# Performance work log

Hardware: AMD Instinct MI355X
Metric: run time of the kernel (lower is better)

The kernel has to match this reference:

```python
import jax, jax.numpy as jnp
import numpy as np

B, NBANDS, NCHAN, NTIME = 32, 9, 64, 4096
M = 32
C = M * NBANDS          # 288 spectral-spatial channels
SF = 4                  # strideFactor
TLEN = 2 * SF - 1       # 7 overlapping temporal windows
E = 2                   # embed_dim
H = 2                   # num_heads (head_dim = 1)
NCLASS = 4
BN_EPS = 1e-5


def _renorm(w, maxnorm):
    # torch.renorm(p=2, dim=0): clamp L2 norm of each dim-0 slice to maxnorm
    norms = jnp.sqrt(jnp.sum(w.reshape(w.shape[0], -1) ** 2, axis=1))
    scale = jnp.minimum(1.0, maxnorm / jnp.maximum(norms, 1e-7))
    return w * scale.reshape((-1,) + (1,) * (w.ndim - 1))


def _pos_embed():
    # get_1d_sincos_pos_embed_from_grid(embed_dim=2, len=7)
    pos = np.arange(TLEN, dtype=np.float32)
    omega = 1.0 / (10000.0 ** (np.arange(E // 2, dtype=np.float32) / (E / 2.0)))
    out = pos[:, None] * omega[None, :]
    return jnp.asarray(np.concatenate([np.sin(out), np.cos(out)], axis=1), jnp.float32)  # [TLEN, E]


def setup_inputs() -> dict:
    key = jax.random.key(0)
    ks = jax.random.split(key, 10)
    s = 0.1
    return {
        "x": jax.random.uniform(ks[0], (B, NBANDS, NCHAN, NTIME), jnp.float32),
        "conv_w": jax.random.normal(ks[1], (C, 1, NCHAN, 1), jnp.float32) * s,
        "conv_b": jax.random.normal(ks[2], (C,), jnp.float32) * s,
        "bn_gamma": jnp.ones((C,), jnp.float32),
        "bn_beta": jnp.zeros((C,), jnp.float32),
        "bn_mean": jnp.zeros((C,), jnp.float32),
        "bn_var": jnp.ones((C,), jnp.float32),
        "in_proj_w": jax.random.normal(ks[3], (C, 3 * E, E), jnp.float32) * s,
        "in_proj_b": jax.random.normal(ks[4], (C, 3 * E), jnp.float32) * s,
        "out_proj_w": jax.random.normal(ks[5], (C, E, E), jnp.float32) * s,
        "out_proj_b": jax.random.normal(ks[6], (C, E), jnp.float32) * s,
        "last_w": jax.random.normal(ks[7], (NCLASS, C * TLEN * E), jnp.float32) * s,
        "last_b": jax.random.normal(ks[8], (NCLASS,), jnp.float32) * s,
    }


def _forward(x, conv_w, conv_b, bn_gamma, bn_beta, bn_mean, bn_var,
             in_proj_w, in_proj_b, out_proj_w, out_proj_b, last_w, last_b):
    # --- SCB: grouped conv (nChan,1) + BatchNorm(eval) + swish ---
    w = _renorm(conv_w, 2.0)
    y = jax.lax.conv_general_dilated(
        x, w, window_strides=(1, 1), padding='VALID',
        dimension_numbers=('NCHW', 'OIHW', 'NCHW'),
        feature_group_count=NBANDS) + conv_b[None, :, None, None]      # [B,C,1,NTIME]
    y = (y - bn_mean[None, :, None, None]) * jax.lax.rsqrt(bn_var + BN_EPS)[None, :, None, None]
    y = y * bn_gamma[None, :, None, None] + bn_beta[None, :, None, None]
    y = y * jax.nn.sigmoid(y)  # swish

    # --- overlapping temporal windows stacked on dim 2 ---
    ts = NTIME // (SF * 2)
    xs = jnp.concatenate([y[:, :, :, i * ts:(i + 2) * ts] for i in range(TLEN)], axis=2)  # [B,C,TLEN,2ts]

    # --- tempo_layer: log-var, RMS/mean shape factor ---
    var = jnp.log(jnp.clip(jnp.var(xs, axis=3, keepdims=True, ddof=1), 1e-6, 1e6))
    mean_ = jnp.mean(xs, axis=3, keepdims=True)
    x_rms = jnp.sqrt(jnp.mean(xs ** 2, axis=3, keepdims=True))
    feat = jnp.concatenate([var, x_rms / mean_], axis=3)               # [B,C,TLEN,E]

    # --- batched per-channel multihead self-attention (replaces C-way loop) ---
    yq = feat + _pos_embed()[None, None]                               # [B,C,T,E]
    qkv = jnp.einsum('bcte,cfe->bctf', yq, in_proj_w) + in_proj_b[None, :, None, :]
    q, k, v = jnp.split(qkv, 3, axis=3)
    hd = E // H
    q = q.reshape(B, C, TLEN, H, hd)
    k = k.reshape(B, C, TLEN, H, hd)
    v = v.reshape(B, C, TLEN, H, hd)
    scores = jnp.einsum('bcthd,bcshd->bchts', q, k) / jnp.sqrt(jnp.float32(hd))
    att = jax.nn.softmax(scores, axis=-1)
    o = jnp.einsum('bchts,bcshd->bcthd', att, v).reshape(B, C, TLEN, E)
    o = jnp.einsum('bcte,cfe->bctf', o, out_proj_w) + out_proj_b[None, :, None, :]

    # --- classifier with weight-norm constraint + log-softmax ---
    flat = o.reshape(B, C * TLEN * E)
    lw = _renorm(last_w, 0.5)
    logits = flat @ lw.T + last_b
    return jax.nn.log_softmax(logits, axis=1)


def reference(x, conv_w, conv_b, bn_gamma, bn_beta, bn_mean, bn_var,
              in_proj_w, in_proj_b, out_proj_w, out_proj_b, last_w, last_b):
    return _forward(x, conv_w, conv_b, bn_gamma, bn_beta, bn_mean, bn_var,
                    in_proj_w, in_proj_b, out_proj_w, out_proj_b, last_w, last_b)
```

## Files before the change

### kernel.cpp

```cpp
#include <hip/hip_runtime.h>
#include <math.h>

#define BB     32
#define NBANDS 9
#define NCHAN  64
#define NTIME  4096
#define CC     288
#define TLEN   7
#define NSEG   8
#define SEGLEN 512
#define NCLASS 4

#define WS_WF    0
#define WS_BIAS  (WS_WF + CC*NCHAN)
#define WS_S1    (WS_BIAS + CC)
#define WS_S2    (WS_S1 + BB*CC*NSEG)
#define WS_FLAT  (WS_S2 + BB*CC*NSEG)

typedef _Float16 f16;
typedef __attribute__((ext_vector_type(8))) _Float16 f16x8;
typedef __attribute__((ext_vector_type(4))) float floatx4;

__global__ __launch_bounds__(64) void k0_fold(
    const float* __restrict__ cw, const float* __restrict__ cb,
    const float* __restrict__ gam, const float* __restrict__ bet,
    const float* __restrict__ mu, const float* __restrict__ var,
    f16* __restrict__ Wh, f16* __restrict__ Wl, float* __restrict__ biasf) {
  int c = blockIdx.x;
  int h = threadIdx.x;
  int g = c >> 5, cc = c & 31;
  float w = cw[c * NCHAN + h];
  float sq = w * w;
#pragma unroll
  for (int off = 32; off; off >>= 1) sq += __shfl_down(sq, off, 64);
  sq = __shfl(sq, 0, 64);
  float norm = sqrtf(sq);
  float scale = fminf(1.0f, 2.0f / fmaxf(norm, 1e-7f));
  float bns = gam[c] / sqrtf(var[c] + 1e-5f);
  float wf = w * scale * bns;
  f16 hi = (f16)wf;
  f16 lo = (f16)(wf - (float)hi);
  int o = g * (NCHAN * 32) + h * 32 + cc;
  Wh[o] = hi;
  Wl[o] = lo;
  if (h == 0) biasf[c] = (cb[c] - mu[c]) * bns + bet[c];
}

__global__ __launch_bounds__(256, 2) void k1_conv(
    const float* __restrict__ x, const f16* __restrict__ Wh,
    const f16* __restrict__ Wl, const float* __restrict__ biasf,
    float* __restrict__ S1, float* __restrict__ S2) {
  int gid = blockIdx.x;
  int seg = gid & 7;
  int g = (gid >> 3) % NBANDS;
  int b = gid / (NBANDS * NSEG);
  int tid = threadIdx.x;
  int wave = tid >> 6, lane = tid & 63;
  int quad = lane >> 4, li = lane & 15;

  const float* xp = x + (size_t)(b * NBANDS + g) * NCHAN * NTIME;
  const f16* wh = Wh + g * (NCHAN * 32);
  const f16* wl = Wl + g * (NCHAN * 32);

  f16x8 ah[2][2], al[2][2];
#pragma unroll
  for (int mt = 0; mt < 2; ++mt)
#pragma unroll
    for (int kb = 0; kb < 2; ++kb)
#pragma unroll
      for (int j = 0; j < 8; ++j) {
        int idx = (kb * 32 + quad * 8 + j) * 32 + mt * 16 + li;
        ah[mt][kb][j] = wh[idx];
        al[mt][kb][j] = wl[idx];
      }

  float biasr[2][4];
#pragma unroll
  for (int mt = 0; mt < 2; ++mt)
#pragma unroll
    for (int r = 0; r < 4; ++r)
      biasr[mt][r] = biasf[g * 32 + mt * 16 + quad * 4 + r];

  float s1a[2][4], s2a[2][4];
#pragma unroll
  for (int mt = 0; mt < 2; ++mt)
#pragma unroll
    for (int r = 0; r < 4; ++r) { s1a[mt][r] = 0.0f; s2a[mt][r] = 0.0f; }

#pragma unroll 1
  for (int ch = 0; ch < 2; ++ch) {
    int tc = seg * SEGLEN + wave * 128 + ch * 64;
    float4 v4[2][8];
#pragma unroll
    for (int kb = 0; kb < 2; ++kb)
#pragma unroll
      for (int j = 0; j < 8; ++j)
        v4[kb][j] = *(const float4*)(xp + (size_t)(kb * 32 + quad * 8 + j) * NTIME
                                     + tc + li * 4);
#pragma unroll
    for (int tau = 0; tau < 4; ++tau) {
      f16x8 bh[2], bl[2];
#pragma unroll
      for (int kb = 0; kb < 2; ++kb)
#pragma unroll
        for (int j = 0; j < 8; ++j) {
          float v = ((const float*)&v4[kb][j])[tau];
          f16 hi = (f16)v;
          bh[kb][j] = hi;
          bl[kb][j] = (f16)(v - (float)hi);
        }
      floatx4 acc0 = {0.0f, 0.0f, 0.0f, 0.0f};
      floatx4 acc1 = {0.0f, 0.0f, 0.0f, 0.0f};
#pragma unroll
      for (int kb = 0; kb < 2; ++kb) {
        acc0 = __builtin_amdgcn_mfma_f32_16x16x32_f16(ah[0][kb], bh[kb], acc0, 0, 0, 0);
        acc0 = __builtin_amdgcn_mfma_f32_16x16x32_f16(ah[0][kb], bl[kb], acc0, 0, 0, 0);
        acc0 = __builtin_amdgcn_mfma_f32_16x16x32_f16(al[0][kb], bh[kb], acc0, 0, 0, 0);
        acc1 = __builtin_amdgcn_mfma_f32_16x16x32_f16(ah[1][kb], bh[kb], acc1, 0, 0, 0);
        acc1 = __builtin_amdgcn_mfma_f32_16x16x32_f16(ah[1][kb], bl[kb], acc1, 0, 0, 0);
        acc1 = __builtin_amdgcn_mfma_f32_16x16x32_f16(al[1][kb], bh[kb], acc1, 0, 0, 0);
      }
#pragma unroll
      for (int r = 0; r < 4; ++r) {
        float d0 = acc0[r] + biasr[0][r];
        float d1 = acc1[r] + biasr[1][r];
        float y0 = d0 * __builtin_amdgcn_rcpf(1.0f + __expf(-d0));
        float y1 = d1 * __builtin_amdgcn_rcpf(1.0f + __expf(-d1));
        s1a[0][r] += y0; s2a[0][r] = fmaf(y0, y0, s2a[0][r]);
        s1a[1][r] += y1; s2a[1][r] = fmaf(y1, y1, s2a[1][r]);
      }
    }
  }

#pragma unroll
  for (int off = 8; off; off >>= 1) {
#pragma unroll
    for (int mt = 0; mt < 2; ++mt)
#pragma unroll
      for (int r = 0; r < 4; ++r) {
        s1a[mt][r] += __shfl_down(s1a[mt][r], off, 16);
        s2a[mt][r] += __shfl_down(s2a[mt][r], off, 16);
      }
  }

  __shared__ float part[2][32][4];
  if (li == 0) {
#pragma unroll
    for (int mt = 0; mt < 2; ++mt)
#pragma unroll
      for (int r = 0; r < 4; ++r) {
        int c = mt * 16 + quad * 4 + r;
        part[0][c][wave] = s1a[mt][r];
        part[1][c][wave] = s2a[mt][r];
      }
  }
  __syncthreads();
  if (tid < 64) {
    int c = tid >> 1, which = tid & 1;
    float v = part[which][c][0] + part[which][c][1] +
              part[which][c][2] + part[which][c][3];
    size_t o = (size_t)((b * CC) + g * 32 + c) * NSEG + seg;
    if (which == 0) S1[o] = v; else S2[o] = v;
  }
}

__global__ __launch_bounds__(256) void k2_attn(
    const float* __restrict__ S1, const float* __restrict__ S2,
    const float* __restrict__ ipw, const float* __restrict__ ipb,
    const float* __restrict__ opw, const float* __restrict__ opb,
    float* __restrict__ flat) {
  const float PSIN[TLEN] = {0.0f, 0.8414709848f, 0.9092974268f, 0.1411200081f,
                            -0.7568024953f, -0.9589242747f, -0.2794154982f};
  const float PCOS[TLEN] = {1.0f, 0.5403023059f, -0.4161468365f, -0.9899924966f,
                            -0.6536436209f, 0.2836621855f, 0.9601702867f};
  int idx = blockIdx.x * blockDim.x + threadIdx.x;
  if (idx >= BB * CC) return;
  int b = idx / CC, c = idx % CC;
  const float* s1 = S1 + (size_t)(b * CC + c) * NSEG;
  const float* s2 = S2 + (size_t)(b * CC + c) * NSEG;

  float yq[TLEN][2];
#pragma unroll
  for (int t = 0; t < TLEN; ++t) {
    float S1w = s1[t] + s1[t + 1];
    float S2w = s2[t] + s2[t + 1];
    float mean = S1w * (1.0f / 1024.0f);
    float var = (S2w - S1w * S1w * (1.0f / 1024.0f)) * (1.0f / 1023.0f);
    var = fminf(fmaxf(var, 1e-6f), 1e6f);
    float rms = sqrtf(S2w * (1.0f / 1024.0f));
    yq[t][0] = __logf(var) + PSIN[t];
    yq[t][1] = rms / mean + PCOS[t];
  }

  const float* W = ipw + c * 12;
  const float* Bp = ipb + c * 6;
  float q[TLEN][2], k[TLEN][2], v[TLEN][2];
#pragma unroll
  for (int t = 0; t < TLEN; ++t) {
#pragma unroll
    for (int f = 0; f < 6; ++f) {
      float val = W[f * 2 + 0] * yq[t][0] + W[f * 2 + 1] * yq[t][1] + Bp[f];
      if (f < 2) q[t][f] = val;
      else if (f < 4) k[t][f - 2] = val;
      else v[t][f - 4] = val;
    }
  }

  float o[TLEN][2];
#pragma unroll
  for (int h = 0; h < 2; ++h) {
#pragma unroll
    for (int t = 0; t < TLEN; ++t) {
      float sc[TLEN];
      float m = -1e30f;
#pragma unroll
      for (int s = 0; s < TLEN; ++s) {
        sc[s] = q[t][h] * k[s][h];
        m = fmaxf(m, sc[s]);
      }
      float sum = 0.0f, acc = 0.0f;
#pragma unroll
      for (int s = 0; s < TLEN; ++s) {
        float e = __expf(sc[s] - m);
        sum += e;
        acc += e * v[s][h];
      }
      o[t][h] = acc / sum;
    }
  }

  const float* Wo = opw + c * 4;
  const float* Bo = opb + c * 2;
  float* out = flat + (size_t)b * (CC * TLEN * 2) + c * (TLEN * 2);
#pragma unroll
  for (int t = 0; t < TLEN; ++t) {
    out[t * 2 + 0] = Wo[0] * o[t][0] + Wo[1] * o[t][1] + Bo[0];
    out[t * 2 + 1] = Wo[2] * o[t][0] + Wo[3] * o[t][1] + Bo[1];
  }
}

__global__ __launch_bounds__(256) void k3_cls(
    const float* __restrict__ flat, const float* __restrict__ lw,
    const float* __restrict__ lb, float* __restrict__ out) {
  const int FEAT = CC * TLEN * 2;
  int b = blockIdx.x;
  int tid = threadIdx.x;
  const float* f = flat + (size_t)b * FEAT;
  float d[NCLASS] = {0, 0, 0, 0}, n2[NCLASS] = {0, 0, 0, 0};
  for (int j = tid; j < FEAT; j += 256) {
    float fv = f[j];
#pragma unroll
    for (int n = 0; n < NCLASS; ++n) {
      float w = lw[n * FEAT + j];
      d[n] = fmaf(fv, w, d[n]);
      n2[n] = fmaf(w, w, n2[n]);
    }
  }
  __shared__ float red[4][8];
  int lane = tid & 63, wave = tid >> 6;
#pragma unroll
  for (int n = 0; n < NCLASS; ++n) {
#pragma unroll
    for (int off = 32; off; off >>= 1) {
      d[n] += __shfl_down(d[n], off, 64);
      n2[n] += __shfl_down(n2[n], off, 64);
    }
  }
  if (lane == 0) {
#pragma unroll
    for (int n = 0; n < NCLASS; ++n) {
      red[wave][n] = d[n];
      red[wave][n + 4] = n2[n];
    }
  }
  __syncthreads();
  if (tid == 0) {
    float logit[NCLASS];
#pragma unroll
    for (int n = 0; n < NCLASS; ++n) {
      float dn = red[0][n] + red[1][n] + red[2][n] + red[3][n];
      float nn = red[0][n + 4] + red[1][n + 4] + red[2][n + 4] + red[3][n + 4];
      float norm = sqrtf(nn);
      float scale = fminf(1.0f, 0.5f / fmaxf(norm, 1e-7f));
      logit[n] = dn * scale + lb[n];
    }
    float m = fmaxf(fmaxf(logit[0], logit[1]), fmaxf(logit[2], logit[3]));
    float s = 0.0f;
#pragma unroll
    for (int n = 0; n < NCLASS; ++n) s += expf(logit[n] - m);
    float ls = logf(s);
#pragma unroll
    for (int n = 0; n < NCLASS; ++n) out[b * NCLASS + n] = logit[n] - m - ls;
  }
}

extern "C" void kernel_launch(void* const* d_in, const int* in_sizes, int n_in,
                              void* d_out, int out_size, void* d_ws, size_t ws_size,
                              hipStream_t stream) {
  const float* x     = (const float*)d_in[0];
  const float* cw    = (const float*)d_in[1];
  const float* cb    = (const float*)d_in[2];
  const float* gam   = (const float*)d_in[3];
  const float* bet   = (const float*)d_in[4];
  const float* mu    = (const float*)d_in[5];
  const float* var   = (const float*)d_in[6];
  const float* ipw   = (const float*)d_in[7];
  const float* ipb   = (const float*)d_in[8];
  const float* opw   = (const float*)d_in[9];
  const float* opb   = (const float*)d_in[10];
  const float* lw    = (const float*)d_in[11];
  const float* lb    = (const float*)d_in[12];
  float* out = (float*)d_out;

  float* ws = (float*)d_ws;
  f16* Wh = (f16*)(ws + WS_WF);
  f16* Wl = Wh + CC * NCHAN;
  float* biasf = ws + WS_BIAS;
  float* S1    = ws + WS_S1;
  float* S2    = ws + WS_S2;
  float* flat  = ws + WS_FLAT;

  k0_fold<<<CC, 64, 0, stream>>>(cw, cb, gam, bet, mu, var, Wh, Wl, biasf);
  k1_conv<<<BB * NBANDS * NSEG, 256, 0, stream>>>(x, Wh, Wl, biasf, S1, S2);
  k2_attn<<<(BB * CC + 255) / 256, 256, 0, stream>>>(S1, S2, ipw, ipb, opw, opb, flat);
  k3_cls<<<BB, 256, 0, stream>>>(flat, lw, lb, out);
}
```

Measured before the change: 437.8 us.

## Double-buffer conv input through LDS with async global_load_lds prefetch

Replaces the per-wave direct float4 register loads of the input signal with an LDS double-buffered pipeline. Each step prefetches the next 64-sample chunk using global_load_lds while the current chunk is split into fp16 hi/lo parts and fed to MFMA. It also raises the occupancy hint from 2 to 4 blocks per CU. The cost is two barriers per step, a padded LDS layout, and reliance on manual vmcnt waits.

Result: no change. 439.2 us (+0.3%).

```diff
diff --git a/kernel.cpp b/kernel.cpp
--- a/kernel.cpp
+++ b/kernel.cpp
@@ -20,6 +20,15 @@
 typedef _Float16 f16;
 typedef __attribute__((ext_vector_type(8))) _Float16 f16x8;
 typedef __attribute__((ext_vector_type(4))) float floatx4;
+
+#define IBLK 260
+#define BUFF (16 * IBLK)
+
+__device__ __forceinline__ void gl_lds16(const float* g, float* l) {
+  __builtin_amdgcn_global_load_lds(
+      (const __attribute__((address_space(1))) void*)g,
+      (__attribute__((address_space(3))) void*)l, 16, 0, 0);
+}
 
 __global__ __launch_bounds__(64) void k0_fold(
     const float* __restrict__ cw, const float* __restrict__ cb,
@@ -46,21 +55,24 @@
   if (h == 0) biasf[c] = (cb[c] - mu[c]) * bns + bet[c];
 }
 
-__global__ __launch_bounds__(256, 2) void k1_conv(
+__global__ __launch_bounds__(256, 4) void k1_conv(
     const float* __restrict__ x, const f16* __restrict__ Wh,
     const f16* __restrict__ Wl, const float* __restrict__ biasf,
     float* __restrict__ S1, float* __restrict__ S2) {
+  __shared__ float lds[2][BUFF];
+  __shared__ float part[2][32][4];
+
   int gid = blockIdx.x;
   int seg = gid & 7;
   int g = (gid >> 3) % NBANDS;
   int b = gid / (NBANDS * NSEG);
   int tid = threadIdx.x;
-  int wave = tid >> 6, lane = tid & 63;
+  int w = tid >> 6, lane = tid & 63;
   int quad = lane >> 4, li = lane & 15;
 
-  const float* xp = x + (size_t)(b * NBANDS + g) * NCHAN * NTIME;
-  const f16* wh = Wh + g * (NCHAN * 32);
-  const f16* wl = Wl + g * (NCHAN * 32);
+  const float* xp = x + (size_t)(b * NBANDS + g) * NCHAN * NTIME + seg * SEGLEN;
+  const f16* whp = Wh + g * (NCHAN * 32);
+  const f16* wlp = Wl + g * (NCHAN * 32);
 
   f16x8 ah[2][2], al[2][2];
 #pragma unroll
@@ -70,8 +82,8 @@
 #pragma unroll
       for (int j = 0; j < 8; ++j) {
         int idx = (kb * 32 + quad * 8 + j) * 32 + mt * 16 + li;
-        ah[mt][kb][j] = wh[idx];
-        al[mt][kb][j] = wl[idx];
+        ah[mt][kb][j] = whp[idx];
+        al[mt][kb][j] = wlp[idx];
       }
 
   float biasr[2][4];
@@ -87,49 +99,60 @@
 #pragma unroll
     for (int r = 0; r < 4; ++r) { s1a[mt][r] = 0.0f; s2a[mt][r] = 0.0f; }
 
+#pragma unroll
+  for (int i = 0; i < 4; ++i) {
+    int I = w * 4 + i;
+    gl_lds16(xp + (size_t)(I * 4 + quad) * NTIME + li * 4, &lds[0][I * IBLK]);
+  }
+
 #pragma unroll 1
-  for (int ch = 0; ch < 2; ++ch) {
-    int tc = seg * SEGLEN + wave * 128 + ch * 64;
-    float4 v4[2][8];
-#pragma unroll
-    for (int kb = 0; kb < 2; ++kb)
-#pragma unroll
-      for (int j = 0; j < 8; ++j)
-        v4[kb][j] = *(const float4*)(xp + (size_t)(kb * 32 + quad * 8 + j) * NTIME
-                                     + tc + li * 4);
-#pragma unroll
-    for (int tau = 0; tau < 4; ++tau) {
-      f16x8 bh[2], bl[2];
-#pragma unroll
-      for (int kb = 0; kb < 2; ++kb)
-#pragma unroll
-        for (int j = 0; j < 8; ++j) {
-          float v = ((const float*)&v4[kb][j])[tau];
-          f16 hi = (f16)v;
-          bh[kb][j] = hi;
-          bl[kb][j] = (f16)(v - (float)hi);
-        }
-      floatx4 acc0 = {0.0f, 0.0f, 0.0f, 0.0f};
-      floatx4 acc1 = {0.0f, 0.0f, 0.0f, 0.0f};
-#pragma unroll
-      for (int kb = 0; kb < 2; ++kb) {
-        acc0 = __builtin_amdgcn_mfma_f32_16x16x32_f16(ah[0][kb], bh[kb], acc0, 0, 0, 0);
-        acc0 = __builtin_amdgcn_mfma_f32_16x16x32_f16(ah[0][kb], bl[kb], acc0, 0, 0, 0);
-        acc0 = __builtin_amdgcn_mfma_f32_16x16x32_f16(al[0][kb], bh[kb], acc0, 0, 0, 0);
-        acc1 = __builtin_amdgcn_mfma_f32_16x16x32_f16(ah[1][kb], bh[kb], acc1, 0, 0, 0);
-        acc1 = __builtin_amdgcn_mfma_f32_16x16x32_f16(ah[1][kb], bl[kb], acc1, 0, 0, 0);
-        acc1 = __builtin_amdgcn_mfma_f32_16x16x32_f16(al[1][kb], bh[kb], acc1, 0, 0, 0);
-      }
-#pragma unroll
-      for (int r = 0; r < 4; ++r) {
-        float d0 = acc0[r] + biasr[0][r];
-        float d1 = acc1[r] + biasr[1][r];
-        float y0 = d0 * __builtin_amdgcn_rcpf(1.0f + __expf(-d0));
-        float y1 = d1 * __builtin_amdgcn_rcpf(1.0f + __expf(-d1));
-        s1a[0][r] += y0; s2a[0][r] = fmaf(y0, y0, s2a[0][r]);
-        s1a[1][r] += y1; s2a[1][r] = fmaf(y1, y1, s2a[1][r]);
-      }
-    }
+  for (int p = 0; p < 8; ++p) {
+    int cur = p & 1;
+    if (p < 7) {
+#pragma unroll
+      for (int i = 0; i < 4; ++i) {
+        int I = w * 4 + i;
+        gl_lds16(xp + (size_t)(I * 4 + quad) * NTIME + (p + 1) * 64 + li * 4,
+                 &lds[cur ^ 1][I * IBLK]);
+      }
+      asm volatile("s_waitcnt vmcnt(4)" ::: "memory");
+    } else {
+      asm volatile("s_waitcnt vmcnt(0)" ::: "memory");
+    }
+    __syncthreads();
+
+    const float* Lb = lds[cur];
+    floatx4 acc0 = {0.0f, 0.0f, 0.0f, 0.0f};
+    floatx4 acc1 = {0.0f, 0.0f, 0.0f, 0.0f};
+#pragma unroll
+    for (int kb = 0; kb < 2; ++kb) {
+      f16x8 bh, bl;
+#pragma unroll
+      for (int j = 0; j < 8; ++j) {
+        int I = kb * 8 + quad * 2 + (j >> 2);
+        int idx = I * IBLK + (j & 3) * 64 + w * 16 + (li >> 2) * 4 + (li & 3);
+        float v = Lb[idx];
+        f16 hi = (f16)v;
+        bh[j] = hi;
+        bl[j] = (f16)(v - (float)hi);
+      }
+      acc0 = __builtin_amdgcn_mfma_f32_16x16x32_f16(ah[0][kb], bh, acc0, 0, 0, 0);
+      acc0 = __builtin_amdgcn_mfma_f32_16x16x32_f16(ah[0][kb], bl, acc0, 0, 0, 0);
+      acc0 = __builtin_amdgcn_mfma_f32_16x16x32_f16(al[0][kb], bh, acc0, 0, 0, 0);
+      acc1 = __builtin_amdgcn_mfma_f32_16x16x32_f16(ah[1][kb], bh, acc1, 0, 0, 0);
+      acc1 = __builtin_amdgcn_mfma_f32_16x16x32_f16(ah[1][kb], bl, acc1, 0, 0, 0);
+      acc1 = __builtin_amdgcn_mfma_f32_16x16x32_f16(al[1][kb], bh, acc1, 0, 0, 0);
+    }
+#pragma unroll
+    for (int r = 0; r < 4; ++r) {
+      float d0 = acc0[r] + biasr[0][r];
+      float d1 = acc1[r] + biasr[1][r];
+      float y0 = d0 * __builtin_amdgcn_rcpf(1.0f + __expf(-d0));
+      float y1 = d1 * __builtin_amdgcn_rcpf(1.0f + __expf(-d1));
+      s1a[0][r] += y0; s2a[0][r] = fmaf(y0, y0, s2a[0][r]);
+      s1a[1][r] += y1; s2a[1][r] = fmaf(y1, y1, s2a[1][r]);
+    }
+    __syncthreads();
   }
 
 #pragma unroll
@@ -143,15 +166,14 @@
       }
   }
 
-  __shared__ float part[2][32][4];
   if (li == 0) {
 #pragma unroll
     for (int mt = 0; mt < 2; ++mt)
 #pragma unroll
       for (int r = 0; r < 4; ++r) {
         int c = mt * 16 + quad * 4 + r;
-        part[0][c][wave] = s1a[mt][r];
-        part[1][c][wave] = s2a[mt][r];
+        part[0][c][w] = s1a[mt][r];
+        part[1][c][w] = s2a[mt][r];
       }
   }
   __syncthreads();
```
